# Kernel optimization log

Hardware: AMD Instinct MI355X
Metric: run time of the kernel (lower is better)

The kernel has to match this reference:

```python
import jax, jax.numpy as jnp
import numpy as np

B, S, D, NH = 2, 1024, 512, 16  # batch, seq_len, d_model, num_heads (chunk size!)
C = D // NH  # number of chunks produced by torch split(num_heads, dim=-1)


def _split_heads(x):
    # torch: torch.stack(x.split(NH, dim=-1)) -> (C, B, S, NH), chunk i = cols [i*NH:(i+1)*NH]
    b, s, d = x.shape
    return jnp.moveaxis(x.reshape(b, s, C, NH), 2, 0)


def setup_inputs() -> dict:
    key = jax.random.key(0)
    ks = jax.random.split(key, 7)
    mk = lambda k, shp, scale=1.0: (jax.random.normal(k, shp, dtype=jnp.float32) * scale)
    return {
        "Q": mk(ks[0], (B, S, D)),
        "K": mk(ks[1], (B, S, D)),
        "V": mk(ks[2], (B, S, D)),
        "Wq": mk(ks[3], (D, D), D ** -0.5),
        "Wk": mk(ks[4], (D, D), D ** -0.5),
        "Wv": mk(ks[5], (D, D), D ** -0.5),
        "Wo": mk(ks[6], (D, D), D ** -0.5),
    }


def reference(Q, K, V, Wq, Wk, Wv, Wo):
    # bias-free linear projections (torch Linear: x @ W.T)
    q = Q @ Wq.T
    k = K @ Wk.T
    v = V @ Wv.T
    qh, kh, vh = _split_heads(q), _split_heads(k), _split_heads(v)  # (C, B, S, NH)
    # NOTE: scale is sqrt(Q.size(-1)) = sqrt(num_heads), faithful to source
    scale = jnp.sqrt(jnp.asarray(float(NH), dtype=qh.dtype))
    scores = jnp.einsum("cbmh,cbnh->cbmn", qh, kh) / scale  # (C, B, S, S)
    weights = jax.nn.softmax(scores, axis=-1)
    att = jnp.einsum("cbmn,cbnh->cbmh", weights, vh)  # (C, B, S, NH)
    # faithful to torch permute(0,2,1,3) then reshape(batch, -1, d_model)
    out = att.transpose(0, 2, 1, 3).reshape(B, -1, D)
    out = out @ Wo.T
    return (out, weights)
```

## Files before the change

kernel.cpp:

```cpp
#include <hip/hip_runtime.h>
#include <cstdint>
#include <cstddef>


typedef __attribute__((ext_vector_type(8)))  short    short8;
typedef __attribute__((ext_vector_type(4)))  float    f32x4;
typedef __attribute__((ext_vector_type(4)))  unsigned u32x4;

union FragU { u32x4 u; short8 s; };

__device__ __forceinline__ unsigned pk_bf16(float a, float b) {
    unsigned ua = __float_as_uint(a), ub = __float_as_uint(b);
    ua = (ua + 0x7fffu + ((ua >> 16) & 1u)) >> 16;
    ub = (ub + 0x7fffu + ((ub >> 16) & 1u)) >> 16;
    return ua | (ub << 16);
}

__device__ __forceinline__ void gemm_nt_mfma_body(const float* __restrict__ X,
                                                  const float* __restrict__ W,
                                                  float* __restrict__ P)
{
    __shared__ unsigned Xs[128 * 17 * 4];
    __shared__ unsigned Ws[64 * 17 * 4];
    const int t  = threadIdx.x;
    const int m0 = blockIdx.y << 7;
    const int n0 = blockIdx.x << 6;
    const int wave = t >> 6, lane = t & 63;
    const int ml = lane & 15;
    const int g  = lane >> 4;

    f32x4 acc[2][4] = {{{0,0,0,0},{0,0,0,0},{0,0,0,0},{0,0,0,0}},
                       {{0,0,0,0},{0,0,0,0},{0,0,0,0},{0,0,0,0}}};

#pragma unroll 1
    for (int st = 0; st < 4; ++st) {
        if (st) __syncthreads();
#pragma unroll
        for (int rep = 0; rep < 8; ++rep) {
            int f  = rep * 256 + t;
            int kf = f & 15, r = f >> 4;
            const float* xr = X + (size_t)(m0 + r) * 512 + st * 128 + kf * 8;
            float4 a = *(const float4*)xr;
            float4 b = *(const float4*)(xr + 4);
            unsigned* dx = &Xs[(r * 17 + kf) * 4];
            dx[0] = pk_bf16(a.x, a.y); dx[1] = pk_bf16(a.z, a.w);
            dx[2] = pk_bf16(b.x, b.y); dx[3] = pk_bf16(b.z, b.w);
        }
#pragma unroll
        for (int rep = 0; rep < 4; ++rep) {
            int f  = rep * 256 + t;
            int kf = f & 15, r = f >> 4;
            const float* wr = W + (size_t)(n0 + r) * 512 + st * 128 + kf * 8;
            float4 c = *(const float4*)wr;
            float4 d = *(const float4*)(wr + 4);
            unsigned* dw = &Ws[(r * 17 + kf) * 4];
            dw[0] = pk_bf16(c.x, c.y); dw[1] = pk_bf16(c.z, c.w);
            dw[2] = pk_bf16(d.x, d.y); dw[3] = pk_bf16(d.z, d.w);
        }
        __syncthreads();
#pragma unroll
        for (int ks = 0; ks < 4; ++ks) {
            const int kf = ks * 4 + g;
            FragU a0, a1;
            a0.u = *(const u32x4*)&Xs[((wave * 32 + ml) * 17 + kf) * 4];
            a1.u = *(const u32x4*)&Xs[((wave * 32 + 16 + ml) * 17 + kf) * 4];
#pragma unroll
            for (int nf = 0; nf < 4; ++nf) {
                FragU bw;
                bw.u = *(const u32x4*)&Ws[((nf * 16 + ml) * 17 + kf) * 4];
                acc[0][nf] = __builtin_amdgcn_mfma_f32_16x16x32_bf16(
                    a0.s, bw.s, acc[0][nf], 0, 0, 0);
                acc[1][nf] = __builtin_amdgcn_mfma_f32_16x16x32_bf16(
                    a1.s, bw.s, acc[1][nf], 0, 0, 0);
            }
        }
    }
#pragma unroll
    for (int af = 0; af < 2; ++af)
#pragma unroll
        for (int nf = 0; nf < 4; ++nf)
#pragma unroll
            for (int r = 0; r < 4; ++r) {
                const int m = m0 + wave * 32 + af * 16 + g * 4 + r;
                P[(size_t)m * 512 + n0 + nf * 16 + ml] = acc[af][nf][r];
            }
}

__global__ __launch_bounds__(256, 2) void proj3_kernel(
    const float* __restrict__ Q, const float* __restrict__ K, const float* __restrict__ V,
    const float* __restrict__ Wq, const float* __restrict__ Wk, const float* __restrict__ Wv,
    float* __restrict__ q, float* __restrict__ k, float* __restrict__ v)
{
    const float* X; const float* W; float* P;
    if (blockIdx.z == 0)      { X = Q; W = Wq; P = q; }
    else if (blockIdx.z == 1) { X = K; W = Wk; P = k; }
    else                      { X = V; W = Wv; P = v; }
    gemm_nt_mfma_body(X, W, P);
}

__global__ __launch_bounds__(256, 2) void outproj_kernel(
    const float* __restrict__ att, const float* __restrict__ Wo, float* __restrict__ out)
{
    gemm_nt_mfma_body(att, Wo, out);
}

__global__ __launch_bounds__(512)
void attn_mfma_kernel(
    const float* __restrict__ q, const float* __restrict__ k, const float* __restrict__ v,
    float* __restrict__ wts, float* __restrict__ att)
{
    __shared__ unsigned ksF[64 * 128];
    __shared__ unsigned vsT[16][514];
    __shared__ unsigned pbuf[8][16][18];

    const int t     = threadIdx.x;
    const int bid   = blockIdx.x;
    const int strip = bid & 7;
    const int cb    = bid >> 3;
    const int b     = cb & 1;
    const int c     = cb >> 1;
    const int m0b   = strip << 7;

    const float* kb = k + (size_t)b * 524288 + c * 16;
    const float* vb = v + (size_t)b * 524288 + c * 16;

#pragma unroll
    for (int rep = 0; rep < 4; ++rep) {
        int f = rep * 512 + t;
        int n = f >> 1, gg = f & 1;
        const float* kr = kb + (size_t)n * 512 + gg * 8;
        float4 a  = *(const float4*)kr;
        float4 bq = *(const float4*)(kr + 4);
        unsigned* dst = &ksF[(n >> 4) * 128 + ((n & 15) + (gg << 4)) * 4];
        dst[0] = pk_bf16(a.x, a.y);
        dst[1] = pk_bf16(a.z, a.w);
        dst[2] = pk_bf16(bq.x, bq.y);
        dst[3] = pk_bf16(bq.z, bq.w);
    }
#pragma unroll
    for (int rep = 0; rep < 4; ++rep) {
        int f = rep * 512 + t;
        int p = f >> 2, hq = f & 3;
        float4 v0 = *(const float4*)(vb + (size_t)(2 * p)     * 512 + hq * 4);
        float4 v1 = *(const float4*)(vb + (size_t)(2 * p + 1) * 512 + hq * 4);
        vsT[hq * 4 + 0][p] = pk_bf16(v0.x, v1.x);
        vsT[hq * 4 + 1][p] = pk_bf16(v0.y, v1.y);
        vsT[hq * 4 + 2][p] = pk_bf16(v0.z, v1.z);
        vsT[hq * 4 + 3][p] = pk_bf16(v0.w, v1.w);
    }
    __syncthreads();

    const int wave = t >> 6, lane = t & 63;
    const int ml = lane & 15;
    const int g  = lane >> 4;
    const int m0w = m0b + wave * 16;

    FragU qf;
    if (g < 2) {
        const float* qr = q + (size_t)b * 524288
                            + (size_t)(m0w + ml) * 512 + c * 16 + g * 8;
        float4 a  = *(const float4*)qr;
        float4 bq = *(const float4*)(qr + 4);
        qf.u[0] = pk_bf16(a.x * 0.25f, a.y * 0.25f);
        qf.u[1] = pk_bf16(a.z * 0.25f, a.w * 0.25f);
        qf.u[2] = pk_bf16(bq.x * 0.25f, bq.y * 0.25f);
        qf.u[3] = pk_bf16(bq.z * 0.25f, bq.w * 0.25f);
    } else {
        qf.u = (u32x4){0, 0, 0, 0};
    }

    const f32x4 zero4 = {0.f, 0.f, 0.f, 0.f};

    float rs = 0.f;
#pragma unroll 1
    for (int nt = 0; nt < 64; ++nt) {
        FragU ka;
        if (lane < 32) ka.u = *(const u32x4*)&ksF[nt * 128 + lane * 4];
        else           ka.u = (u32x4){0, 0, 0, 0};
        f32x4 st = __builtin_amdgcn_mfma_f32_16x16x32_bf16(ka.s, qf.s, zero4, 0, 0, 0);
        rs += (__expf(st[0]) + __expf(st[1])) + (__expf(st[2]) + __expf(st[3]));
    }
    rs += __shfl_xor(rs, 16);
    rs += __shfl_xor(rs, 32);
    const float inv = 1.0f / rs;

    f32x4 acc = zero4;
    float* wrow = wts + (size_t)cb * 1048576 + (size_t)(m0w + ml) * 1024;
#pragma unroll 1
    for (int ntp = 0; ntp < 32; ++ntp) {
#pragma unroll
        for (int sub = 0; sub < 2; ++sub) {
            const int nt = ntp * 2 + sub;
            FragU ka;
            if (lane < 32) ka.u = *(const u32x4*)&ksF[nt * 128 + lane * 4];
            else           ka.u = (u32x4){0, 0, 0, 0};
            f32x4 st = __builtin_amdgcn_mfma_f32_16x16x32_bf16(ka.s, qf.s, zero4, 0, 0, 0);
            float w0 = __expf(st[0]) * inv;
            float w1 = __expf(st[1]) * inv;
            float w2 = __expf(st[2]) * inv;
            float w3 = __expf(st[3]) * inv;
            *(float4*)(wrow + nt * 16 + g * 4) = make_float4(w0, w1, w2, w3);
            unsigned* pb = &pbuf[wave][ml][sub * 8 + g * 2];
            pb[0] = pk_bf16(w0, w1);
            pb[1] = pk_bf16(w2, w3);
        }
        FragU pa, vf;
        pa.u = *(const u32x4*)&pbuf[wave][ml][g * 4];
        vf.u = *(const u32x4*)&vsT[ml][ntp * 16 + g * 4];
        acc = __builtin_amdgcn_mfma_f32_16x16x32_bf16(pa.s, vf.s, acc, 0, 0, 0);
    }

    const int b2 = c >> 4;
#pragma unroll
    for (int r = 0; r < 4; ++r) {
        const int m  = m0w + g * 4 + r;
        const int m2 = (c & 15) * 64 + (m >> 4);
        const int d2 = (m & 15) * 32 + b * 16 + ml;
        att[((size_t)b2 * 1024 + m2) * 512 + d2] = acc[r];
    }
}

extern "C" void kernel_launch(void* const* d_in, const int* in_sizes, int n_in,
                              void* d_out, int out_size, void* d_ws, size_t ws_size,
                              hipStream_t stream)
{
    (void)in_sizes; (void)n_in; (void)out_size; (void)ws_size;
    const float* Q  = (const float*)d_in[0];
    const float* K  = (const float*)d_in[1];
    const float* V  = (const float*)d_in[2];
    const float* Wq = (const float*)d_in[3];
    const float* Wk = (const float*)d_in[4];
    const float* Wv = (const float*)d_in[5];
    const float* Wo = (const float*)d_in[6];

    float* out = (float*)d_out;
    float* wts = out + 1048576;

    float* ws  = (float*)d_ws;
    float* q   = ws;
    float* k   = ws + (1u << 20);
    float* v   = ws + 2 * (1u << 20);
    float* att = ws + 3 * (1u << 20);

    proj3_kernel<<<dim3(8, 16, 3), 256, 0, stream>>>(Q, K, V, Wq, Wk, Wv, q, k, v);
    attn_mfma_kernel<<<512, 512, 0, stream>>>(q, k, v, wts, att);
    outproj_kernel<<<dim3(8, 16, 1), 256, 0, stream>>>(att, Wo, out);
}
```

Baseline: 103.3 us.

## Store q/k/v projections as bf16 and fold query scale into Wq

The projection kernel now writes q, k and v as bf16 instead of fp32, and the 1/sqrt(NH) query scale is folded into the Wq tile during staging. The attention kernel then loads bf16 directly into its fragments and shared memory with no per-element conversion. This halves the intermediate write and read traffic and removes conversion ALU work from the attention kernel. The attention kernel re-reads K/V once per strip, so the saving is multiplied. Rounding is unchanged because the values were already converted to bf16 before the MFMA, but the query is now scaled before rounding rather than after.

```diff
diff --git a/kernel.cpp b/kernel.cpp
--- a/kernel.cpp
+++ b/kernel.cpp
@@ -15,10 +15,16 @@
     ub = (ub + 0x7fffu + ((ub >> 16) & 1u)) >> 16;
     return ua | (ub << 16);
 }
-
+__device__ __forceinline__ unsigned short bf16_1(float a) {
+    unsigned ua = __float_as_uint(a);
+    return (unsigned short)((ua + 0x7fffu + ((ua >> 16) & 1u)) >> 16);
+}
+
+template <bool BF16OUT>
 __device__ __forceinline__ void gemm_nt_mfma_body(const float* __restrict__ X,
                                                   const float* __restrict__ W,
-                                                  float* __restrict__ P)
+                                                  void* __restrict__ Pout,
+                                                  float wscale)
 {
     __shared__ unsigned Xs[128 * 17 * 4];
     __shared__ unsigned Ws[64 * 17 * 4];
@@ -54,8 +60,10 @@
             float4 c = *(const float4*)wr;
             float4 d = *(const float4*)(wr + 4);
             unsigned* dw = &Ws[(r * 17 + kf) * 4];
-            dw[0] = pk_bf16(c.x, c.y); dw[1] = pk_bf16(c.z, c.w);
-            dw[2] = pk_bf16(d.x, d.y); dw[3] = pk_bf16(d.z, d.w);
+            dw[0] = pk_bf16(c.x * wscale, c.y * wscale);
+            dw[1] = pk_bf16(c.z * wscale, c.w * wscale);
+            dw[2] = pk_bf16(d.x * wscale, d.y * wscale);
+            dw[3] = pk_bf16(d.z * wscale, d.w * wscale);
         }
         __syncthreads();
 #pragma unroll
@@ -82,31 +90,37 @@
 #pragma unroll
             for (int r = 0; r < 4; ++r) {
                 const int m = m0 + wave * 32 + af * 16 + g * 4 + r;
-                P[(size_t)m * 512 + n0 + nf * 16 + ml] = acc[af][nf][r];
+                const size_t idx = (size_t)m * 512 + n0 + nf * 16 + ml;
+                if (BF16OUT)
+                    ((unsigned short*)Pout)[idx] = bf16_1(acc[af][nf][r]);
+                else
+                    ((float*)Pout)[idx] = acc[af][nf][r];
             }
 }
 
 __global__ __launch_bounds__(256, 2) void proj3_kernel(
     const float* __restrict__ Q, const float* __restrict__ K, const float* __restrict__ V,
     const float* __restrict__ Wq, const float* __restrict__ Wk, const float* __restrict__ Wv,
-    float* __restrict__ q, float* __restrict__ k, float* __restrict__ v)
-{
-    const float* X; const float* W; float* P;
-    if (blockIdx.z == 0)      { X = Q; W = Wq; P = q; }
-    else if (blockIdx.z == 1) { X = K; W = Wk; P = k; }
-    else                      { X = V; W = Wv; P = v; }
-    gemm_nt_mfma_body(X, W, P);
+    unsigned short* __restrict__ q, unsigned short* __restrict__ k,
+    unsigned short* __restrict__ v)
+{
+    const float* X; const float* W; unsigned short* P; float ws;
+    if (blockIdx.z == 0)      { X = Q; W = Wq; P = q; ws = 0.25f; }
+    else if (blockIdx.z == 1) { X = K; W = Wk; P = k; ws = 1.0f; }
+    else                      { X = V; W = Wv; P = v; ws = 1.0f; }
+    gemm_nt_mfma_body<true>(X, W, P, ws);
 }
 
 __global__ __launch_bounds__(256, 2) void outproj_kernel(
     const float* __restrict__ att, const float* __restrict__ Wo, float* __restrict__ out)
 {
-    gemm_nt_mfma_body(att, Wo, out);
+    gemm_nt_mfma_body<false>(att, Wo, out, 1.0f);
 }
 
 __global__ __launch_bounds__(512)
 void attn_mfma_kernel(
-    const float* __restrict__ q, const float* __restrict__ k, const float* __restrict__ v,
+    const unsigned short* __restrict__ q, const unsigned short* __restrict__ k,
+    const unsigned short* __restrict__ v,
     float* __restrict__ wts, float* __restrict__ att)
 {
     __shared__ unsigned ksF[64 * 128];
@@ -121,32 +135,26 @@
     const int c     = cb >> 1;
     const int m0b   = strip << 7;
 
-    const float* kb = k + (size_t)b * 524288 + c * 16;
-    const float* vb = v + (size_t)b * 524288 + c * 16;
+    const unsigned short* kb = k + (size_t)b * 524288 + c * 16;
+    const unsigned short* vb = v + (size_t)b * 524288 + c * 16;
 
 #pragma unroll
     for (int rep = 0; rep < 4; ++rep) {
         int f = rep * 512 + t;
         int n = f >> 1, gg = f & 1;
-        const float* kr = kb + (size_t)n * 512 + gg * 8;
-        float4 a  = *(const float4*)kr;
-        float4 bq = *(const float4*)(kr + 4);
-        unsigned* dst = &ksF[(n >> 4) * 128 + ((n & 15) + (gg << 4)) * 4];
-        dst[0] = pk_bf16(a.x, a.y);
-        dst[1] = pk_bf16(a.z, a.w);
-        dst[2] = pk_bf16(bq.x, bq.y);
-        dst[3] = pk_bf16(bq.z, bq.w);
+        u32x4 kv = *(const u32x4*)(kb + (size_t)n * 512 + gg * 8);
+        *(u32x4*)&ksF[(n >> 4) * 128 + ((n & 15) + (gg << 4)) * 4] = kv;
     }
 #pragma unroll
     for (int rep = 0; rep < 4; ++rep) {
         int f = rep * 512 + t;
         int p = f >> 2, hq = f & 3;
-        float4 v0 = *(const float4*)(vb + (size_t)(2 * p)     * 512 + hq * 4);
-        float4 v1 = *(const float4*)(vb + (size_t)(2 * p + 1) * 512 + hq * 4);
-        vsT[hq * 4 + 0][p] = pk_bf16(v0.x, v1.x);
-        vsT[hq * 4 + 1][p] = pk_bf16(v0.y, v1.y);
-        vsT[hq * 4 + 2][p] = pk_bf16(v0.z, v1.z);
-        vsT[hq * 4 + 3][p] = pk_bf16(v0.w, v1.w);
+        uint2 a  = *(const uint2*)(vb + (size_t)(2 * p)     * 512 + hq * 4);
+        uint2 bb = *(const uint2*)(vb + (size_t)(2 * p + 1) * 512 + hq * 4);
+        vsT[hq * 4 + 0][p] = (a.x & 0xffffu) | (bb.x << 16);
+        vsT[hq * 4 + 1][p] = (a.x >> 16) | (bb.x & 0xffff0000u);
+        vsT[hq * 4 + 2][p] = (a.y & 0xffffu) | (bb.y << 16);
+        vsT[hq * 4 + 3][p] = (a.y >> 16) | (bb.y & 0xffff0000u);
     }
     __syncthreads();
 
@@ -157,14 +165,8 @@
 
     FragU qf;
     if (g < 2) {
-        const float* qr = q + (size_t)b * 524288
-                            + (size_t)(m0w + ml) * 512 + c * 16 + g * 8;
-        float4 a  = *(const float4*)qr;
-        float4 bq = *(const float4*)(qr + 4);
-        qf.u[0] = pk_bf16(a.x * 0.25f, a.y * 0.25f);
-        qf.u[1] = pk_bf16(a.z * 0.25f, a.w * 0.25f);
-        qf.u[2] = pk_bf16(bq.x * 0.25f, bq.y * 0.25f);
-        qf.u[3] = pk_bf16(bq.z * 0.25f, bq.w * 0.25f);
+        qf.u = *(const u32x4*)(q + (size_t)b * 524288
+                                 + (size_t)(m0w + ml) * 512 + c * 16 + g * 8);
     } else {
         qf.u = (u32x4){0, 0, 0, 0};
     }
@@ -237,12 +239,13 @@
     float* wts = out + 1048576;
 
     float* ws  = (float*)d_ws;
-    float* q   = ws;
-    float* k   = ws + (1u << 20);
-    float* v   = ws + 2 * (1u << 20);
-    float* att = ws + 3 * (1u << 20);
-
-    proj3_kernel<<<dim3(8, 16, 3), 256, 0, stream>>>(Q, K, V, Wq, Wk, Wv, q, k, v);
-    attn_mfma_kernel<<<512, 512, 0, stream>>>(q, k, v, wts, att);
+    unsigned short* q16 = (unsigned short*)ws;
+    unsigned short* k16 = (unsigned short*)(ws + (1u << 19));
+    unsigned short* v16 = (unsigned short*)(ws + (1u << 20));
+    float* att = ws + 2 * (1u << 20);
+
+    proj3_kernel<<<dim3(8, 16, 3), 256, 0, stream>>>(Q, K, V, Wq, Wk, Wv,
+                                                     q16, k16, v16);
+    attn_mfma_kernel<<<512, 512, 0, stream>>>(q16, k16, v16, wts, att);
     outproj_kernel<<<dim3(8, 16, 1), 256, 0, stream>>>(att, Wo, out);
 }
```

Measured after the change: 97.56 us (median of 2 runs). 5.5% less time.
